# Performance work log

Measured on AMD Instinct MI355X. Metric: run time of the kernel, lower is better.

The kernel has to match this reference:

```python
import jax, jax.numpy as jnp
import numpy as np

SCENE = (60, 36, 60)          # int(4.8/0.08), int(2.88/0.08), int(4.8/0.08)
VOX = 0.08
DS = 4
IMG_W, IMG_H = 640, 480
N_VOX = SCENE[0] * SCENE[1] * SCENE[2]

def _voxel_grid():
    gx, gy, gz = np.meshgrid(np.arange(SCENE[0]), np.arange(SCENE[1]), np.arange(SCENE[2]), indexing='ij')
    return np.stack([gx.ravel(), gy.ravel(), gz.ravel()], axis=1).astype(np.float32)  # [N,3]

_GRID = jnp.asarray(_voxel_grid())


def setup_inputs() -> dict:
    key = jax.random.key(0)
    x2d = jax.random.normal(jax.random.fold_in(key, 0), (512, IMG_H // DS, IMG_W // DS), dtype=jnp.float32)
    inv_cam_pose = jnp.eye(4, dtype=jnp.float32)
    vox_origin = jnp.array([-2.4, -2.4, 0.1], dtype=jnp.float32)
    cam_k = jnp.array([[518.8579, 0.0, 320.0], [0.0, 518.8579, 240.0], [0.0, 0.0, 1.0]], dtype=jnp.float32)
    old_voxel_indices = jax.random.randint(jax.random.fold_in(key, 1), (1000, 3), 0, 60)
    old_image_indices = jax.random.randint(jax.random.fold_in(key, 2), (1000, 2), 0, 480)
    return {"x2d": x2d, "inv_cam_pose": inv_cam_pose, "vox_origin": vox_origin, "cam_k": cam_k,
            "old_voxel_indices": old_voxel_indices, "old_image_indices": old_image_indices, "fliplr": 0}


def reference(x2d, inv_cam_pose, vox_origin, cam_k, old_voxel_indices, old_image_indices, fliplr):
    # old_voxel_indices / old_image_indices are unused in the original forward.
    c, h, w = x2d.shape
    grid = _GRID                                        # [N,3] voxel integer coords (float)
    pts_world2 = grid * VOX + 0.5 * VOX                 # voxel centers
    # axis swap: world (x, z, y) then shift by origin
    pts_world = jnp.stack([pts_world2[:, 0], pts_world2[:, 2], pts_world2[:, 1]], axis=1) + vox_origin[None, :]
    homo = jnp.concatenate([pts_world, jnp.ones((pts_world.shape[0], 1), pts_world.dtype)], axis=1)
    pts_cam = homo @ inv_cam_pose.T                     # [N,4] camera frame
    in_front = pts_cam[:, 2] > 0
    pts_img = pts_cam[:, :3] @ cam_k.T                  # [N,3]
    uv = jnp.round(pts_img[:, :2] / pts_img[:, 2:3])    # [N,2] = (x_col, y_row)
    in_frustum = (uv[:, 0] >= 0) & (uv[:, 0] < IMG_W) & (uv[:, 1] >= 0) & (uv[:, 1] < IMG_H)
    mask = in_front & in_frustum

    row, col = uv[:, 1], uv[:, 0]                       # torch.fliplr -> (y, x)
    if fliplr:
        col = IMG_W - 1 - col
    row = jnp.floor(row / DS)                           # // downsample
    col = jnp.floor(col / DS)
    lin_img = jnp.where(mask, (row * w + col), 0.0).astype(jnp.int32)  # safe gather index

    src = x2d.reshape(c, -1)
    feats = src[:, lin_img]                             # [c, N] gather

    lin_vox = (grid[:, 0] * (SCENE[1] * SCENE[2]) + grid[:, 1] * SCENE[2] + grid[:, 2]).astype(jnp.int32)
    lin_vox = jnp.where(mask, lin_vox, N_VOX)           # out-of-range -> dropped
    x3d = jnp.zeros((c, N_VOX), x2d.dtype).at[:, lin_vox].set(feats, mode='drop')
    return x3d.reshape(c, SCENE[0], SCENE[1], SCENE[2])
```

## Files before the change

kernel.cpp:

```cpp
#include <hip/hip_runtime.h>

#define NVOX 129600
#define NCH  512
#define NPIX 19200
#define IMW  160

__global__ __launch_bounds__(256) void transpose_kernel(
    const float* __restrict__ x2d, float* __restrict__ xT)
{
    __shared__ float tile[64][65];
    int p0 = blockIdx.x * 64;
    int c0 = blockIdx.y * 64;
    int t  = threadIdx.x;
    int a  = t & 15;
    int bq = t >> 4;

    const float4* src4 = reinterpret_cast<const float4*>(x2d);
#pragma unroll
    for (int i = 0; i < 4; ++i) {
        int c = bq + i * 16;
        float4 v = src4[((size_t)(c0 + c) * NPIX + p0) / 4 + a];
        tile[a * 4 + 0][c] = v.x;
        tile[a * 4 + 1][c] = v.y;
        tile[a * 4 + 2][c] = v.z;
        tile[a * 4 + 3][c] = v.w;
    }
    __syncthreads();
    float4* dst4 = reinterpret_cast<float4*>(xT);
#pragma unroll
    for (int i = 0; i < 4; ++i) {
        int p = bq + i * 16;
        float4 v;
        v.x = tile[p][a * 4 + 0];
        v.y = tile[p][a * 4 + 1];
        v.z = tile[p][a * 4 + 2];
        v.w = tile[p][a * 4 + 3];
        dst4[((size_t)(p0 + p) * NCH + c0) / 4 + a] = v;
    }
}

__global__ __launch_bounds__(512) void gather_kernel(
    const float* __restrict__ xT,
    const float* __restrict__ pose,
    const float* __restrict__ origin,
    const float* __restrict__ camk,
    const int*   __restrict__ fliplr,
    float*       __restrict__ out)
{
    __shared__ float lds[64 * 130];
    __shared__ int   lin_s[64];

    int b    = blockIdx.x;
    int q    = b & 3;
    int vb   = b >> 2;
    int v0   = vb * 64;
    int c0   = q * 128;
    int t    = threadIdx.x;
    int wv   = t >> 6;
    int lane = t & 63;

    if (t < 64) {
        int v  = v0 + t;
        int gx = v / 2160;
        int r  = v - gx * 2160;
        int gy = r / 60;
        int gz = r - gy * 60;
        float wx = gx * 0.08f + 0.04f + origin[0];
        float wy = gz * 0.08f + 0.04f + origin[1];
        float wz = gy * 0.08f + 0.04f + origin[2];
        float cx = pose[0]*wx + pose[1]*wy + pose[2]*wz  + pose[3];
        float cy = pose[4]*wx + pose[5]*wy + pose[6]*wz  + pose[7];
        float cz = pose[8]*wx + pose[9]*wy + pose[10]*wz + pose[11];
        float ix = camk[0]*cx + camk[1]*cy + camk[2]*cz;
        float iy = camk[3]*cx + camk[4]*cy + camk[5]*cz;
        float iz = camk[6]*cx + camk[7]*cy + camk[8]*cz;
        float u  = rintf(ix / iz);
        float vv = rintf(iy / iz);
        bool ok = (cz > 0.0f) && (u >= 0.0f) && (u < 640.0f)
                              && (vv >= 0.0f) && (vv < 480.0f);
        int l = -1;
        if (ok) {
            float colf = fliplr[0] ? (639.0f - u) : u;
            l = (((int)vv) >> 2) * IMW + (((int)colf) >> 2);
        }
        lin_s[t] = l;
    }
    __syncthreads();

#pragma unroll
    for (int k = 0; k < 8; ++k) {
        int w = wv * 8 + k;
        int l = lin_s[w];
        if (l >= 0) {
            const float2* src = reinterpret_cast<const float2*>(
                xT + (size_t)l * NCH + c0);
            float2 val = src[lane];
            *reinterpret_cast<float2*>(&lds[w * 130 + lane * 2]) = val;
        }
    }
    __syncthreads();

    int  myl   = lin_s[lane];
    bool valid = myl >= 0;
    float* obase = out + (size_t)c0 * NVOX + v0 + lane;
#pragma unroll
    for (int i = 0; i < 16; ++i) {
        int cc = wv * 16 + i;
        float val = valid ? lds[lane * 130 + cc] : 0.0f;
        __builtin_nontemporal_store(val, &obase[(size_t)cc * NVOX]);
    }
}

__global__ __launch_bounds__(256) void fused_kernel(
    const float* __restrict__ x2d, const float* __restrict__ pose,
    const float* __restrict__ origin, const float* __restrict__ camk,
    const int* __restrict__ fliplr, float* __restrict__ out)
{
    long tid = (long)blockIdx.x * blockDim.x + threadIdx.x;
    int g  = (int)(tid % 32400);
    int cg = (int)(tid / 32400);
    if (cg >= 64) return;
    int v0 = g * 4;
    int lin[4];
#pragma unroll
    for (int i = 0; i < 4; ++i) {
        int v = v0 + i;
        int gx = v / 2160; int r = v - gx * 2160;
        int gy = r / 60;   int gz = r - gy * 60;
        float wx = gx * 0.08f + 0.04f + origin[0];
        float wy = gz * 0.08f + 0.04f + origin[1];
        float wz = gy * 0.08f + 0.04f + origin[2];
        float cx = pose[0]*wx + pose[1]*wy + pose[2]*wz  + pose[3];
        float cy = pose[4]*wx + pose[5]*wy + pose[6]*wz  + pose[7];
        float cz = pose[8]*wx + pose[9]*wy + pose[10]*wz + pose[11];
        float ix = camk[0]*cx + camk[1]*cy + camk[2]*cz;
        float iy = camk[3]*cx + camk[4]*cy + camk[5]*cz;
        float iz = camk[6]*cx + camk[7]*cy + camk[8]*cz;
        float u  = rintf(ix / iz);
        float vv = rintf(iy / iz);
        bool ok = (cz > 0.0f) && (u >= 0.0f) && (u < 640.0f)
                              && (vv >= 0.0f) && (vv < 480.0f);
        int l = -1;
        if (ok) {
            float colf = fliplr[0] ? (639.0f - u) : u;
            l = (((int)vv) >> 2) * IMW + (((int)colf) >> 2);
        }
        lin[i] = l;
    }
    int ch0 = cg * 8;
#pragma unroll
    for (int cc = 0; cc < 8; ++cc) {
        int ch = ch0 + cc;
        const float* s = x2d + (size_t)ch * NPIX;
        float4 o;
        o.x = (lin[0] >= 0) ? s[lin[0]] : 0.0f;
        o.y = (lin[1] >= 0) ? s[lin[1]] : 0.0f;
        o.z = (lin[2] >= 0) ? s[lin[2]] : 0.0f;
        o.w = (lin[3] >= 0) ? s[lin[3]] : 0.0f;
        *reinterpret_cast<float4*>(out + (size_t)ch * NVOX + v0) = o;
    }
}

extern "C" void kernel_launch(void* const* d_in, const int* in_sizes, int n_in,
                              void* d_out, int out_size, void* d_ws, size_t ws_size,
                              hipStream_t stream) {
    const float* x2d    = (const float*)d_in[0];
    const float* pose   = (const float*)d_in[1];
    const float* origin = (const float*)d_in[2];
    const float* camk   = (const float*)d_in[3];
    const int*   flip   = (const int*)d_in[6];
    float*       out    = (float*)d_out;

    const size_t xT_bytes = (size_t)NPIX * NCH * sizeof(float);
    if (ws_size >= xT_bytes) {
        float* xT = (float*)d_ws;
        transpose_kernel<<<dim3(NPIX / 64, NCH / 64), dim3(256), 0, stream>>>(x2d, xT);
        gather_kernel<<<dim3((NVOX / 64) * 4), dim3(512), 0, stream>>>(
            xT, pose, origin, camk, flip, out);
    } else {
        fused_kernel<<<dim3(8100), dim3(256), 0, stream>>>(
            x2d, pose, origin, camk, flip, out);
    }
}
```

Before: 68.29 us.

## Precompute voxel projections in transpose pass; retile gather to 256 voxels x 32 channels

Moves the per-voxel projection into the transpose kernel and writes a lin-index buffer to workspace, so the gather kernel no longer recomputes projections for every channel quarter. The gather is retiled to 256 voxels by 32 channels per block, reads float4 from the transposed source and writes float4 nontemporal stores to the output rows. The aim is to cut redundant projection math (previously 4x per voxel) and widen output stores. The cost is extra workspace traffic for the index buffer, more blocks with smaller channel slices, and a dependency on the lin buffer being 16-byte aligned for the int4 loads.

Result: slower. 69.97 us (+2.5%).

```diff
diff --git a/kernel.cpp b/kernel.cpp
--- a/kernel.cpp
+++ b/kernel.cpp
@@ -4,14 +4,57 @@
 #define NCH  512
 #define NPIX 19200
 #define IMW  160
+#define VB   256
+#define CB   32
+#define LSTR 260
+#define NQ   (NCH / CB)
+#define NVB  ((NVOX + VB - 1) / VB)
 
-__global__ __launch_bounds__(256) void transpose_kernel(
-    const float* __restrict__ x2d, float* __restrict__ xT)
+typedef float vfloat4 __attribute__((ext_vector_type(4)));
+
+__device__ __forceinline__ int project_voxel(
+    int v, const float* __restrict__ pose, const float* __restrict__ origin,
+    const float* __restrict__ camk, int flip)
 {
+    int gx = v / 2160;
+    int r  = v - gx * 2160;
+    int gy = r / 60;
+    int gz = r - gy * 60;
+    float wx = gx * 0.08f + 0.04f + origin[0];
+    float wy = gz * 0.08f + 0.04f + origin[1];
+    float wz = gy * 0.08f + 0.04f + origin[2];
+    float cx = pose[0]*wx + pose[1]*wy + pose[2]*wz  + pose[3];
+    float cy = pose[4]*wx + pose[5]*wy + pose[6]*wz  + pose[7];
+    float cz = pose[8]*wx + pose[9]*wy + pose[10]*wz + pose[11];
+    float ix = camk[0]*cx + camk[1]*cy + camk[2]*cz;
+    float iy = camk[3]*cx + camk[4]*cy + camk[5]*cz;
+    float iz = camk[6]*cx + camk[7]*cy + camk[8]*cz;
+    float u  = rintf(ix / iz);
+    float vv = rintf(iy / iz);
+    bool ok = (cz > 0.0f) && (u >= 0.0f) && (u < 640.0f)
+                          && (vv >= 0.0f) && (vv < 480.0f);
+    if (!ok) return -1;
+    float colf = flip ? (639.0f - u) : u;
+    return ((((int)vv) >> 2) * IMW) + (((int)colf) >> 2);
+}
+
+__global__ __launch_bounds__(256) void transpose_proj_kernel(
+    const float* __restrict__ x2d, float* __restrict__ xT,
+    int* __restrict__ lin,
+    const float* __restrict__ pose, const float* __restrict__ origin,
+    const float* __restrict__ camk, const int* __restrict__ fliplr)
+{
+    int bid = blockIdx.y * gridDim.x + blockIdx.x;
+    int t   = threadIdx.x;
+    if (bid < NVB) {
+        int v = bid * 256 + t;
+        if (v < NVOX)
+            lin[v] = project_voxel(v, pose, origin, camk, fliplr[0]);
+    }
+
     __shared__ float tile[64][65];
     int p0 = blockIdx.x * 64;
     int c0 = blockIdx.y * 64;
-    int t  = threadIdx.x;
     int a  = t & 15;
     int bq = t >> 4;
 
@@ -40,74 +83,56 @@
 }
 
 __global__ __launch_bounds__(512) void gather_kernel(
-    const float* __restrict__ xT,
-    const float* __restrict__ pose,
-    const float* __restrict__ origin,
-    const float* __restrict__ camk,
-    const int*   __restrict__ fliplr,
-    float*       __restrict__ out)
+    const float* __restrict__ xT, const int* __restrict__ lin,
+    float* __restrict__ out)
 {
-    __shared__ float lds[64 * 130];
-    __shared__ int   lin_s[64];
+    __shared__ float lds[CB * LSTR];
 
-    int b    = blockIdx.x;
-    int q    = b & 3;
-    int vb   = b >> 2;
-    int v0   = vb * 64;
-    int c0   = q * 128;
-    int t    = threadIdx.x;
-    int wv   = t >> 6;
-    int lane = t & 63;
+    int b  = blockIdx.x;
+    int q  = b & (NQ - 1);
+    int vb = b >> 4;
+    int v0 = vb * VB;
+    int c0 = q * CB;
+    int nv = min(VB, NVOX - v0);
+    int t  = threadIdx.x;
 
-    if (t < 64) {
-        int v  = v0 + t;
-        int gx = v / 2160;
-        int r  = v - gx * 2160;
-        int gy = r / 60;
-        int gz = r - gy * 60;
-        float wx = gx * 0.08f + 0.04f + origin[0];
-        float wy = gz * 0.08f + 0.04f + origin[1];
-        float wz = gy * 0.08f + 0.04f + origin[2];
-        float cx = pose[0]*wx + pose[1]*wy + pose[2]*wz  + pose[3];
-        float cy = pose[4]*wx + pose[5]*wy + pose[6]*wz  + pose[7];
-        float cz = pose[8]*wx + pose[9]*wy + pose[10]*wz + pose[11];
-        float ix = camk[0]*cx + camk[1]*cy + camk[2]*cz;
-        float iy = camk[3]*cx + camk[4]*cy + camk[5]*cz;
-        float iz = camk[6]*cx + camk[7]*cy + camk[8]*cz;
-        float u  = rintf(ix / iz);
-        float vv = rintf(iy / iz);
-        bool ok = (cz > 0.0f) && (u >= 0.0f) && (u < 640.0f)
-                              && (vv >= 0.0f) && (vv < 480.0f);
-        int l = -1;
-        if (ok) {
-            float colf = fliplr[0] ? (639.0f - u) : u;
-            l = (((int)vv) >> 2) * IMW + (((int)colf) >> 2);
-        }
-        lin_s[t] = l;
-    }
-    __syncthreads();
-
+    const float4* xT4 = reinterpret_cast<const float4*>(xT);
 #pragma unroll
-    for (int k = 0; k < 8; ++k) {
-        int w = wv * 8 + k;
-        int l = lin_s[w];
-        if (l >= 0) {
-            const float2* src = reinterpret_cast<const float2*>(
-                xT + (size_t)l * NCH + c0);
-            float2 val = src[lane];
-            *reinterpret_cast<float2*>(&lds[w * 130 + lane * 2]) = val;
+    for (int i = 0; i < 4; ++i) {
+        int r  = i * 64 + (t >> 3);
+        int c4 = (t & 7) * 4;
+        if (r < nv) {
+            int l = lin[v0 + r];
+            if (l >= 0) {
+                float4 val = xT4[((size_t)l * NCH + c0 + c4) >> 2];
+                lds[(c4 + 0) * LSTR + r] = val.x;
+                lds[(c4 + 1) * LSTR + r] = val.y;
+                lds[(c4 + 2) * LSTR + r] = val.z;
+                lds[(c4 + 3) * LSTR + r] = val.w;
+            }
         }
     }
     __syncthreads();
 
-    int  myl   = lin_s[lane];
-    bool valid = myl >= 0;
-    float* obase = out + (size_t)c0 * NVOX + v0 + lane;
+    int wv = t >> 6, lane = t & 63;
+    int vq = lane * 4;
+    int4 lv = make_int4(-1, -1, -1, -1);
+    if (vq < nv)
+        lv = reinterpret_cast<const int4*>(lin + v0)[lane];
 #pragma unroll
-    for (int i = 0; i < 16; ++i) {
-        int cc = wv * 16 + i;
-        float val = valid ? lds[lane * 130 + cc] : 0.0f;
-        __builtin_nontemporal_store(val, &obase[(size_t)cc * NVOX]);
+    for (int i = 0; i < 4; ++i) {
+        int cc = i * 8 + wv;
+        if (vq < nv) {
+            const float* row = &lds[cc * LSTR + vq];
+            float4 d = *reinterpret_cast<const float4*>(row);
+            vfloat4 o;
+            o.x = (lv.x >= 0) ? d.x : 0.0f;
+            o.y = (lv.y >= 0) ? d.y : 0.0f;
+            o.z = (lv.z >= 0) ? d.z : 0.0f;
+            o.w = (lv.w >= 0) ? d.w : 0.0f;
+            __builtin_nontemporal_store(o, reinterpret_cast<vfloat4*>(
+                out + (size_t)(c0 + cc) * NVOX + v0 + vq));
+        }
     }
 }
 
@@ -121,42 +146,20 @@
     int cg = (int)(tid / 32400);
     if (cg >= 64) return;
     int v0 = g * 4;
-    int lin[4];
+    int linv[4];
 #pragma unroll
-    for (int i = 0; i < 4; ++i) {
-        int v = v0 + i;
-        int gx = v / 2160; int r = v - gx * 2160;
-        int gy = r / 60;   int gz = r - gy * 60;
-        float wx = gx * 0.08f + 0.04f + origin[0];
-        float wy = gz * 0.08f + 0.04f + origin[1];
-        float wz = gy * 0.08f + 0.04f + origin[2];
-        float cx = pose[0]*wx + pose[1]*wy + pose[2]*wz  + pose[3];
-        float cy = pose[4]*wx + pose[5]*wy + pose[6]*wz  + pose[7];
-        float cz = pose[8]*wx + pose[9]*wy + pose[10]*wz + pose[11];
-        float ix = camk[0]*cx + camk[1]*cy + camk[2]*cz;
-        float iy = camk[3]*cx + camk[4]*cy + camk[5]*cz;
-        float iz = camk[6]*cx + camk[7]*cy + camk[8]*cz;
-        float u  = rintf(ix / iz);
-        float vv = rintf(iy / iz);
-        bool ok = (cz > 0.0f) && (u >= 0.0f) && (u < 640.0f)
-                              && (vv >= 0.0f) && (vv < 480.0f);
-        int l = -1;
-        if (ok) {
-            float colf = fliplr[0] ? (639.0f - u) : u;
-            l = (((int)vv) >> 2) * IMW + (((int)colf) >> 2);
-        }
-        lin[i] = l;
-    }
+    for (int i = 0; i < 4; ++i)
+        linv[i] = project_voxel(v0 + i, pose, origin, camk, fliplr[0]);
     int ch0 = cg * 8;
 #pragma unroll
     for (int cc = 0; cc < 8; ++cc) {
         int ch = ch0 + cc;
         const float* s = x2d + (size_t)ch * NPIX;
         float4 o;
-        o.x = (lin[0] >= 0) ? s[lin[0]] : 0.0f;
-        o.y = (lin[1] >= 0) ? s[lin[1]] : 0.0f;
-        o.z = (lin[2] >= 0) ? s[lin[2]] : 0.0f;
-        o.w = (lin[3] >= 0) ? s[lin[3]] : 0.0f;
+        o.x = (linv[0] >= 0) ? s[linv[0]] : 0.0f;
+        o.y = (linv[1] >= 0) ? s[linv[1]] : 0.0f;
+        o.z = (linv[2] >= 0) ? s[linv[2]] : 0.0f;
+        o.w = (linv[3] >= 0) ? s[linv[3]] : 0.0f;
         *reinterpret_cast<float4*>(out + (size_t)ch * NVOX + v0) = o;
     }
 }
@@ -171,12 +174,14 @@
     const int*   flip   = (const int*)d_in[6];
     float*       out    = (float*)d_out;
 
-    const size_t xT_bytes = (size_t)NPIX * NCH * sizeof(float);
-    if (ws_size >= xT_bytes) {
-        float* xT = (float*)d_ws;
-        transpose_kernel<<<dim3(NPIX / 64, NCH / 64), dim3(256), 0, stream>>>(x2d, xT);
-        gather_kernel<<<dim3((NVOX / 64) * 4), dim3(512), 0, stream>>>(
-            xT, pose, origin, camk, flip, out);
+    const size_t xT_bytes  = (size_t)NPIX * NCH * sizeof(float);
+    const size_t lin_bytes = (size_t)NVB * VB * sizeof(int);
+    if (ws_size >= xT_bytes + lin_bytes) {
+        float* xT   = (float*)d_ws;
+        int*   linb = (int*)((char*)d_ws + xT_bytes);
+        transpose_proj_kernel<<<dim3(NPIX / 64, NCH / 64), dim3(256), 0, stream>>>(
+            x2d, xT, linb, pose, origin, camk, flip);
+        gather_kernel<<<dim3(NVB * NQ), dim3(512), 0, stream>>>(xT, linb, out);
     } else {
         fused_kernel<<<dim3(8100), dim3(256), 0, stream>>>(
             x2d, pose, origin, camk, flip, out);
```
